# Kernel optimization log

Hardware: AMD Instinct MI355X
Metric: run time of the kernel (lower is better)

## Reference

```python
import jax, jax.numpy as jnp
import numpy as np

B, T_IN, D = 16, 2048, 384
OUT_LEN = 4096  # == max over batch of sum(repeat_count), enforced in setup_inputs


def setup_inputs() -> dict:
    key = jax.random.key(0)
    kx, kr = jax.random.split(key)
    x = jax.random.normal(kx, (B, T_IN, D), dtype=jnp.float32)
    r = jax.random.randint(kr, (B, T_IN), 0, 4, dtype=jnp.int32)
    # cap each row's cumulative sum at OUT_LEN, then force row 0 to hit OUT_LEN
    # exactly so that int(max(sum(repeat_count))) == OUT_LEN (static shape).
    c = jnp.minimum(jnp.cumsum(r, axis=-1), OUT_LEN)
    r = jnp.diff(c, prepend=0, axis=-1)
    r = r.at[0, -1].add(OUT_LEN - c[0, -1])
    return {"x": x, "repeat_count": r.astype(jnp.int32),
            "output_max_seq_len": OUT_LEN}


def reference(x, repeat_count, output_max_seq_len):
    # Torch module builds a one-hot expansion matrix M [B, T_out, T_in] and does
    # bmm(M, x). Equivalently: output frame p of batch b copies input token j
    # where j = searchsorted(cumsum(repeat_count[b]), p, side='right'),
    # and frames p >= sum(repeat_count[b]) are zero (rows of M left as zeros).
    cum = jnp.cumsum(repeat_count, axis=-1)          # [B, T_in]
    output_seq_len = cum[:, -1]                      # [B]
    pos = jnp.arange(output_max_seq_len)             # [T_out]
    # per-batch gather indices  [B, T_out]
    idx = jax.vmap(lambda c: jnp.searchsorted(c, pos, side='right'))(cum)
    idx = jnp.clip(idx, 0, x.shape[1] - 1)
    out = jnp.take_along_axis(x, idx[..., None], axis=1)  # [B, T_out, D]
    valid = (pos[None, :] < output_seq_len[:, None])       # [B, T_out]
    out = out * valid[:, :, None].astype(x.dtype)
    return out, output_seq_len
```

## Files before the change

kernel.cpp:

```cpp
#include <hip/hip_runtime.h>

#define NB      16
#define T_IN    2048
#define OUT_LEN 4096
#define D       384
#define D4      (D / 4)

typedef float f32x4 __attribute__((ext_vector_type(4)));

__global__ __launch_bounds__(256) void cumsum_kernel(const int* __restrict__ r,
                                                     int* __restrict__ cum,
                                                     float* __restrict__ seqlen_out) {
    const int b   = blockIdx.x;
    const int tid = threadIdx.x;
    const int4* rb = (const int4*)(r + b * T_IN);
    int4*       cb = (int4*)(cum + b * T_IN);

    int4 v0 = rb[tid * 2];
    int4 v1 = rb[tid * 2 + 1];
    int v[8] = {v0.x, v0.y, v0.z, v0.w, v1.x, v1.y, v1.z, v1.w};

    int s = 0;
#pragma unroll
    for (int i = 0; i < 8; ++i) { s += v[i]; v[i] = s; }

    const int lane = tid & 63;
    const int wid  = tid >> 6;
    int pre = s;
#pragma unroll
    for (int off = 1; off < 64; off <<= 1) {
        int up = __shfl_up(pre, off, 64);
        if (lane >= off) pre += up;
    }

    __shared__ int wsum[4];
    if (lane == 63) wsum[wid] = pre;
    __syncthreads();

    int excl = pre - s;
    for (int w = 0; w < wid; ++w) excl += wsum[w];

#pragma unroll
    for (int i = 0; i < 8; ++i) v[i] += excl;

    cb[tid * 2]     = make_int4(v[0], v[1], v[2], v[3]);
    cb[tid * 2 + 1] = make_int4(v[4], v[5], v[6], v[7]);

    if (tid == 255) seqlen_out[b] = (float)v[7];
}

__global__ __launch_bounds__(256) void regulate_kernel(const f32x4* __restrict__ x,
                                                       const int* __restrict__ cum,
                                                       f32x4* __restrict__ out) {
    const unsigned row0 = blockIdx.x * 8u;
    const unsigned b    = row0 >> 12;
    const int* cb = cum + b * T_IN;

    __shared__ int sidx[8];
    if (threadIdx.x < 8) {
        const int t   = (int)(row0 & (OUT_LEN - 1)) + (int)threadIdx.x;
        const int seq = cb[T_IN - 1];
        int res = -1;
        if (t < seq) {
            int lo = 0, hi = T_IN;
            while (lo < hi) {
                int mid = (lo + hi) >> 1;
                if (cb[mid] <= t) lo = mid + 1; else hi = mid;
            }
            res = lo < (T_IN - 1) ? lo : (T_IN - 1);
        }
        sidx[threadIdx.x] = res;
    }
    __syncthreads();

    const f32x4*  xb   = x + (size_t)b * T_IN * D4;
    const unsigned base = row0 * (unsigned)D4;

#pragma unroll
    for (int k = 0; k < 3; ++k) {
        const unsigned local = threadIdx.x + k * 256u;
        const unsigned rloc  = local / D4;
        const unsigned d     = local - rloc * D4;
        const int irow = sidx[rloc];
        f32x4 val = (f32x4)(0.f);
        if (irow >= 0) val = xb[(unsigned)irow * D4 + d];
        __builtin_nontemporal_store(val, &out[base + local]);
    }
}

extern "C" void kernel_launch(void* const* d_in, const int* in_sizes, int n_in,
                              void* d_out, int out_size, void* d_ws, size_t ws_size,
                              hipStream_t stream) {
    const float* x  = (const float*)d_in[0];
    const int*   rc = (const int*)d_in[1];

    float* out        = (float*)d_out;
    float* seqlen_out = out + (size_t)NB * OUT_LEN * D;

    int* cum = (int*)d_ws;

    cumsum_kernel<<<NB, 256, 0, stream>>>(rc, cum, seqlen_out);

    const unsigned n_rows = (unsigned)NB * OUT_LEN;
    regulate_kernel<<<n_rows / 8, 256, 0, stream>>>((const f32x4*)x, cum,
                                                    (f32x4*)out);
}
```

Measured before the change: 158.0 us.

## Fuse cumsum into regulate kernel and recompute prefix sum per block

Merges the two kernels into one: every block loads its batch's repeat counts, builds the prefix sum in shared memory, and binary-searches there instead of reading global cum. This removes one launch and the serial dependency between kernels. The cost is that each of the 8192 blocks redundantly scans 2048 ints (8KB read plus LDS scan) and uses 8KB of LDS. The output store also changes from nontemporal to a regular store.

```diff
diff --git a/kernel.cpp b/kernel.cpp
--- a/kernel.cpp
+++ b/kernel.cpp
@@ -8,14 +8,19 @@
 
 typedef float f32x4 __attribute__((ext_vector_type(4)));
 
-__global__ __launch_bounds__(256) void cumsum_kernel(const int* __restrict__ r,
-                                                     int* __restrict__ cum,
+__global__ __launch_bounds__(256) void lenreg_kernel(const f32x4* __restrict__ x,
+                                                     const int* __restrict__ r,
+                                                     f32x4* __restrict__ out,
                                                      float* __restrict__ seqlen_out) {
-    const int b   = blockIdx.x;
+    __shared__ int scum[T_IN];
+    __shared__ int wsum[4];
+    __shared__ int sidx[8];
+
+    const unsigned row0 = blockIdx.x * 8u;
+    const unsigned b    = row0 >> 12;
     const int tid = threadIdx.x;
+
     const int4* rb = (const int4*)(r + b * T_IN);
-    int4*       cb = (int4*)(cum + b * T_IN);
-
     int4 v0 = rb[tid * 2];
     int4 v1 = rb[tid * 2 + 1];
     int v[8] = {v0.x, v0.y, v0.z, v0.w, v1.x, v1.y, v1.z, v1.w};
@@ -32,45 +37,34 @@
         int up = __shfl_up(pre, off, 64);
         if (lane >= off) pre += up;
     }
-
-    __shared__ int wsum[4];
     if (lane == 63) wsum[wid] = pre;
     __syncthreads();
 
     int excl = pre - s;
     for (int w = 0; w < wid; ++w) excl += wsum[w];
-
 #pragma unroll
     for (int i = 0; i < 8; ++i) v[i] += excl;
 
-    cb[tid * 2]     = make_int4(v[0], v[1], v[2], v[3]);
-    cb[tid * 2 + 1] = make_int4(v[4], v[5], v[6], v[7]);
+    ((int4*)scum)[tid * 2]     = make_int4(v[0], v[1], v[2], v[3]);
+    ((int4*)scum)[tid * 2 + 1] = make_int4(v[4], v[5], v[6], v[7]);
+    __syncthreads();
 
-    if (tid == 255) seqlen_out[b] = (float)v[7];
-}
-
-__global__ __launch_bounds__(256) void regulate_kernel(const f32x4* __restrict__ x,
-                                                       const int* __restrict__ cum,
-                                                       f32x4* __restrict__ out) {
-    const unsigned row0 = blockIdx.x * 8u;
-    const unsigned b    = row0 >> 12;
-    const int* cb = cum + b * T_IN;
-
-    __shared__ int sidx[8];
-    if (threadIdx.x < 8) {
-        const int t   = (int)(row0 & (OUT_LEN - 1)) + (int)threadIdx.x;
-        const int seq = cb[T_IN - 1];
+    const int seq = scum[T_IN - 1];
+    if (tid < 8) {
+        const int t = (int)(row0 & (OUT_LEN - 1)) + tid;
         int res = -1;
         if (t < seq) {
             int lo = 0, hi = T_IN;
             while (lo < hi) {
                 int mid = (lo + hi) >> 1;
-                if (cb[mid] <= t) lo = mid + 1; else hi = mid;
+                if (scum[mid] <= t) lo = mid + 1; else hi = mid;
             }
             res = lo < (T_IN - 1) ? lo : (T_IN - 1);
         }
-        sidx[threadIdx.x] = res;
+        sidx[tid] = res;
     }
+    if (tid == 0 && (row0 & (OUT_LEN - 1)) == 0)
+        seqlen_out[b] = (float)seq;
     __syncthreads();
 
     const f32x4*  xb   = x + (size_t)b * T_IN * D4;
@@ -78,13 +72,13 @@
 
 #pragma unroll
     for (int k = 0; k < 3; ++k) {
-        const unsigned local = threadIdx.x + k * 256u;
+        const unsigned local = (unsigned)tid + k * 256u;
         const unsigned rloc  = local / D4;
         const unsigned d     = local - rloc * D4;
         const int irow = sidx[rloc];
         f32x4 val = (f32x4)(0.f);
         if (irow >= 0) val = xb[(unsigned)irow * D4 + d];
-        __builtin_nontemporal_store(val, &out[base + local]);
+        out[base + local] = val;
     }
 }
 
@@ -97,11 +91,7 @@
     float* out        = (float*)d_out;
     float* seqlen_out = out + (size_t)NB * OUT_LEN * D;
 
-    int* cum = (int*)d_ws;
-
-    cumsum_kernel<<<NB, 256, 0, stream>>>(rc, cum, seqlen_out);
-
     const unsigned n_rows = (unsigned)NB * OUT_LEN;
-    regulate_kernel<<<n_rows / 8, 256, 0, stream>>>((const f32x4*)x, cum,
-                                                    (f32x4*)out);
+    lenreg_kernel<<<n_rows / 8, 256, 0, stream>>>((const f32x4*)x, rc,
+                                                  (f32x4*)out, seqlen_out);
 }
```

New measurement: 144.0 us. 8.8% less time.
